# Kernel tuning notes

Hardware: AMD Instinct MI355X
Metric: run time of the kernel (lower is better)

The kernel has to match this reference:

```python
import jax, jax.numpy as jnp
import numpy as np

DECAY = 0.99
EPS_VQ = 1e-5
EPS_LN = 1e-5


def setup_inputs() -> dict:
    key = jax.random.key(0)
    ks = jax.random.split(key, 6)
    N, DIN, D, K = 32768, 1024, 512, 1024
    return {
        "x": jax.random.normal(ks[0], (N, DIN), dtype=jnp.float32),
        "enc_w": jax.random.normal(ks[1], (DIN, D), dtype=jnp.float32) * (1.0 / np.sqrt(DIN)),
        "enc_b": jnp.zeros((D,), jnp.float32),
        "ln_g": jnp.ones((D,), jnp.float32),
        "ln_b": jnp.zeros((D,), jnp.float32),
        "dec_w": jax.random.normal(ks[2], (D, DIN), dtype=jnp.float32) * (1.0 / np.sqrt(D)),
        "dec_b": jnp.zeros((DIN,), jnp.float32),
        "embeddings": jax.random.normal(ks[3], (K, D), dtype=jnp.float32),
        "cluster_size": jnp.ones((K,), jnp.float32),
        "ema_embed_sum": jax.random.normal(ks[4], (K, D), dtype=jnp.float32),
    }


def _layernorm(h, g, b):
    mu = jnp.mean(h, axis=-1, keepdims=True)
    var = jnp.var(h, axis=-1, keepdims=True)
    return (h - mu) * jax.lax.rsqrt(var + EPS_LN) * g + b


def reference(x, enc_w, enc_b, ln_g, ln_b, dec_w, dec_b, embeddings, cluster_size, ema_embed_sum):
    K = embeddings.shape[0]
    # encoder: Linear + LayerNorm
    z_e = _layernorm(x @ enc_w + enc_b, ln_g, ln_b)  # [N, D]
    # pairwise squared L2 distances, expanded GEMM form (same argmin as (z-e)^2.sum)
    d = (jnp.sum(z_e * z_e, axis=1, keepdims=True)
         - 2.0 * (z_e @ embeddings.T)
         + jnp.sum(embeddings * embeddings, axis=1)[None, :])  # [N, K]
    indices = jnp.argmin(d, axis=1)  # [N]
    z_q = embeddings[indices]  # gather [N, D]
    # EMA codebook update (training path; buffers, no grad)
    zd = jax.lax.stop_gradient(z_e)
    counts = jax.ops.segment_sum(jnp.ones_like(indices, jnp.float32), indices, num_segments=K)
    embed_sum = jax.ops.segment_sum(zd, indices, num_segments=K)  # one_hot.T @ z
    new_cluster_size = DECAY * cluster_size + (1.0 - DECAY) * counts
    new_ema_embed_sum = DECAY * ema_embed_sum + (1.0 - DECAY) * embed_sum
    n = jnp.sum(new_cluster_size)
    cs = (new_cluster_size + EPS_VQ) / (n + K * EPS_VQ) * n
    new_embeddings = new_ema_embed_sum / cs[:, None]
    # commitment loss + straight-through estimator
    commit_loss = jnp.mean((z_e - jax.lax.stop_gradient(z_q)) ** 2)
    z_q_st = z_e + jax.lax.stop_gradient(z_q - z_e)
    x_recon = z_q_st @ dec_w + dec_b
    return (x_recon, commit_loss, indices, z_e, z_q_st,
            new_embeddings, new_cluster_size, new_ema_embed_sum)
```

## Files before the change

### kernel.cpp

```cpp
#include <hip/hip_runtime.h>

typedef unsigned long long u64;
typedef unsigned int u32;
typedef _Float16 f16;
typedef _Float16 f16x8 __attribute__((ext_vector_type(8)));
typedef float f32x4 __attribute__((ext_vector_type(4)));

#define MFMA16(a, b, c) __builtin_amdgcn_mfma_f32_16x16x32_f16(a, b, c, 0, 0, 0)

#define NROWS 32768
#define DIN   1024
#define DM    512
#define KC    1024
#define SPLIT_SC  1024.0f
#define SPLIT_INV 0.0009765625f
#define CHSZ  32
#define MAXCH 2048
#define MARGIN 0.5f

#define OFF_XR   0ull
#define OFF_CL   33554432ull
#define OFF_IDX  33554433ull
#define OFF_ZE   33587201ull
#define OFF_ZQ   50364417ull
#define OFF_NE   67141633ull
#define OFF_NCS  67665921ull
#define OFF_NEMA 67666945ull

#define WS_ZNORM   2359296ull
#define WS_IDX     2490368ull
#define WS_COUNTS  2621440ull
#define WS_STARTS  2625536ull
#define WS_OFFW    2629632ull
#define WS_ROWLIST 2633728ull
#define WS_CSD     2764800ull
#define WS_ENORM   2769920ull
#define WS2_CAND   (4ull<<20)
#define WS2_WT1    (36ull<<20)
#define WS2_WT2    (37ull<<20)
#define WS2_DT     (38ull<<20)
#define WS2_E1     (39ull<<20)
#define WS3_CHPFX  (41ull<<20)
#define WS3_CHCODE ((41ull<<20) + 8192)
#define WS3_CPART  ((41ull<<20) + 16384)
#define WS3_PART   ((41ull<<20) + 65536)

__device__ inline void gload16(const f16* g, f16* l) {
  __builtin_amdgcn_global_load_lds((const __attribute__((address_space(1))) void*)g,
                                   (__attribute__((address_space(3))) void*)l, 16, 0, 0);
}

__device__ inline f16x8 ldfrag32(const f16* p, int row, int kc) {
  return *(const f16x8*)(p + row * 32 + ((kc ^ ((row >> 1) & 3)) << 3));
}
__device__ inline f16x8 ldfrag64(const f16* p, int row, int kc) {
  return *(const f16x8*)(p + row * 64 + ((kc ^ (row & 7)) << 3));
}

__device__ inline void stage32(const f16* gbase, int ld, int row0, int k0,
                               f16* lds, int t) {
  int r = t >> 2, c = t & 3;
  int cs = c ^ ((r >> 1) & 3);
  gload16(gbase + (size_t)(row0 + r) * ld + k0 + cs * 8, lds + t * 8);
}

__device__ inline void stage64(const f16* gbase, int ld, int row0, int k0,
                               f16* lds, int t) {
#pragma unroll
  for (int h = 0; h < 2; h++) {
    int e = t + h * 512;
    int r = e >> 3, c = e & 7;
    int cs = c ^ (r & 7);
    gload16(gbase + (size_t)(row0 + r) * ld + k0 + cs * 8, lds + e * 8);
  }
}

#define BAR1_V4   { asm volatile("s_waitcnt vmcnt(4)" ::: "memory"); \
                    __builtin_amdgcn_sched_barrier(0); \
                    __builtin_amdgcn_s_barrier(); \
                    asm volatile("" ::: "memory"); }
#define BAR1_V0L0 { asm volatile("s_waitcnt vmcnt(0) lgkmcnt(0)" ::: "memory"); \
                    __builtin_amdgcn_sched_barrier(0); \
                    __builtin_amdgcn_s_barrier(); \
                    asm volatile("" ::: "memory"); }
#define BAR2      { asm volatile("s_waitcnt lgkmcnt(0)" ::: "memory"); \
                    __builtin_amdgcn_s_barrier(); \
                    asm volatile("" ::: "memory"); }

__device__ inline u32 enc_score(float s) {
  u32 kb = __float_as_uint(s);
  return (kb & 0x80000000u) ? ~kb : (kb | 0x80000000u);
}
__device__ inline float dec_score(u32 u) {
  u32 b = (u & 0x80000000u) ? (u & 0x7fffffffu) : ~u;
  return __uint_as_float(b);
}

__global__ __launch_bounds__(256) void k_init(int* __restrict__ counts) {
  int i = blockIdx.x * 256 + threadIdx.x;
  if (i < KC) counts[i] = 0;
}

__global__ __launch_bounds__(256) void k_prept(const float* __restrict__ W,
                                               f16* __restrict__ o1,
                                               f16* __restrict__ o2,
                                               int K, int N) {
  __shared__ float tile[32][33];
  int tx = threadIdx.x & 31, ty = threadIdx.x >> 5;
  int nb = blockIdx.x * 32, kb = blockIdx.y * 32;
#pragma unroll
  for (int i = 0; i < 32; i += 8)
    tile[ty + i][tx] = W[(size_t)(kb + ty + i) * N + nb + tx];
  __syncthreads();
#pragma unroll
  for (int i = 0; i < 32; i += 8) {
    float v = tile[tx][ty + i];
    f16 h = (f16)v;
    size_t o = (size_t)(nb + ty + i) * K + kb + tx;
    o1[o] = h;
    if (o2) o2[o] = (f16)((v - (float)h) * SPLIT_SC);
  }
}

__global__ __launch_bounds__(256) void k_prepe(const float* __restrict__ E,
                                               f16* __restrict__ e1) {
  int tid = blockIdx.x * 256 + threadIdx.x;
  for (int i = tid; i < KC * DM; i += 131072) e1[i] = (f16)E[i];
}

__global__ __launch_bounds__(64) void k_enorm(const float* __restrict__ E,
                                              float* __restrict__ enorm) {
  int k = blockIdx.x, t = threadIdx.x;
  float s = 0.f;
#pragma unroll
  for (int j = 0; j < 8; j++) {
    float v = E[(size_t)k * DM + t + j * 64];
    s = fmaf(v, v, s);
  }
#pragma unroll
  for (int m = 1; m < 64; m <<= 1) s += __shfl_xor(s, m, 64);
  if (t == 0) enorm[k] = s;
}

__global__ __launch_bounds__(512) void k_genc2(const float* __restrict__ x,
                                               const f16* __restrict__ wt1,
                                               const f16* __restrict__ wt2,
                                               const float* __restrict__ bias,
                                               float* __restrict__ dst) {
  __shared__ __align__(16) f16 A1[128 * 32], A2[128 * 32];
  __shared__ __align__(16) f16 B1[2][128 * 32], B2[2][128 * 32];
  int t = threadIdx.x, lane = t & 63, wid = t >> 6;
  int wm = wid >> 2, wn = wid & 3;
  int l = blockIdx.x;
  int xcd = l & 7, s = l >> 3, ct = s & 3;
  int p = ((s >> 2) << 3) | xcd;
  int m0 = p * 128, n0 = ct * 128;
  int r = t >> 2, cg = t & 3;
  int cslot = cg ^ ((r >> 1) & 3);
  const float* ax = x + (size_t)(m0 + r) * DIN + cg * 8;
  f32x4 accA[4][2] = {}, accB[4][2] = {};

  float4 av0 = *(const float4*)(ax);
  float4 av1 = *(const float4*)(ax + 4);
  stage32(wt1, DIN, n0, 0, B1[0], t);
  stage32(wt2, DIN, n0, 0, B2[0], t);
  int cur = 0;

  for (int it = 0; it < 32; ++it) {
    float4 nv0 = av0, nv1 = av1;
    if (it < 31) {
      int k0n = (it + 1) * 32;
      stage32(wt1, DIN, n0, k0n, B1[cur ^ 1], t);
      stage32(wt2, DIN, n0, k0n, B2[cur ^ 1], t);
      nv0 = *(const float4*)(ax + k0n);
      nv1 = *(const float4*)(ax + k0n + 4);
      asm volatile("s_waitcnt vmcnt(4)" ::: "memory");
    } else {
      asm volatile("s_waitcnt vmcnt(0)" ::: "memory");
    }
    {
      float a[8] = {av0.x, av0.y, av0.z, av0.w, av1.x, av1.y, av1.z, av1.w};
      f16 h1[8], h2[8];
#pragma unroll
      for (int j = 0; j < 8; j++) {
        f16 h = (f16)a[j];
        h1[j] = h;
        h2[j] = (f16)((a[j] - (float)h) * SPLIT_SC);
      }
      *(f16x8*)(A1 + r * 32 + cslot * 8) = *(f16x8*)h1;
      *(f16x8*)(A2 + r * 32 + cslot * 8) = *(f16x8*)h2;
    }
    asm volatile("s_waitcnt lgkmcnt(0)" ::: "memory");
    __builtin_amdgcn_sched_barrier(0);
    __builtin_amdgcn_s_barrier();
    asm volatile("" ::: "memory");
    {
      int kc = lane >> 4;
      f16x8 a1f[4], a2f[4], b1f[2], b2f[2];
#pragma unroll
      for (int m = 0; m < 4; m++) {
        int row = wm * 64 + m * 16 + (lane & 15);
        a1f[m] = ldfrag32(A1, row, kc);
        a2f[m] = ldfrag32(A2, row, kc);
      }
#pragma unroll
      for (int n = 0; n < 2; n++) {
        int row = wn * 32 + n * 16 + (lane & 15);
        b1f[n] = ldfrag32(B1[cur], row, kc);
        b2f[n] = ldfrag32(B2[cur], row, kc);
      }
#pragma unroll
      for (int m = 0; m < 4; m++)
#pragma unroll
        for (int n = 0; n < 2; n++) {
          accA[m][n] = MFMA16(a1f[m], b1f[n], accA[m][n]);
          accB[m][n] = MFMA16(a1f[m], b2f[n], accB[m][n]);
          accB[m][n] = MFMA16(a2f[m], b1f[n], accB[m][n]);
        }
    }
    BAR2;
    av0 = nv0; av1 = nv1; cur ^= 1;
  }
#pragma unroll
  for (int m = 0; m < 4; m++)
#pragma unroll
    for (int n = 0; n < 2; n++)
#pragma unroll
      for (int j = 0; j < 4; j++) {
        int row = m0 + wm * 64 + m * 16 + (lane >> 4) * 4 + j;
        int col = n0 + wn * 32 + n * 16 + (lane & 15);
        dst[(size_t)row * DM + col] = accA[m][n][j] + SPLIT_INV * accB[m][n][j] + bias[col];
      }
}

__global__ __launch_bounds__(512) void k_dist3(const f16* __restrict__ z1,
                                               const f16* __restrict__ e1,
                                               const float* __restrict__ enorm,
                                               u64* __restrict__ cand) {
  __shared__ __align__(16) f16 A1[2][128 * 64], B1[2][128 * 64];
  __shared__ u64 cand_s[128][8];
  int t = threadIdx.x, lane = t & 63, wid = t >> 6;
  int wm = wid >> 2, wn = wid & 3;
  int l = blockIdx.x;
  int xcd = l & 7, s = l >> 3, ct = s & 7;
  int p = ((s >> 3) << 3) | xcd;
  int r0 = p * 128, c0 = ct * 128;
  f32x4 acc[4][2] = {};

  stage64(z1, DM, r0, 0, A1[0], t);
  stage64(e1, DM, c0, 0, B1[0], t);
  int cur = 0;

  for (int it = 0; it < 8; ++it) {
    if (it < 7) {
      int k0n = (it + 1) * 64;
      stage64(z1, DM, r0, k0n, A1[cur ^ 1], t);
      stage64(e1, DM, c0, k0n, B1[cur ^ 1], t);
      BAR1_V4;
    } else {
      BAR1_V0L0;
    }
#pragma unroll
    for (int kk = 0; kk < 2; kk++) {
      int kc = kk * 4 + (lane >> 4);
      f16x8 a1f[4], b1f[2];
#pragma unroll
      for (int m = 0; m < 4; m++)
        a1f[m] = ldfrag64(A1[cur], wm * 64 + m * 16 + (lane & 15), kc);
#pragma unroll
      for (int n = 0; n < 2; n++)
        b1f[n] = ldfrag64(B1[cur], wn * 32 + n * 16 + (lane & 15), kc);
#pragma unroll
      for (int m = 0; m < 4; m++)
#pragma unroll
        for (int n = 0; n < 2; n++) acc[m][n] = MFMA16(a1f[m], b1f[n], acc[m][n]);
    }
    BAR2;
    cur ^= 1;
  }

  float en0 = enorm[c0 + wn * 32 + (lane & 15)];
  float en1 = enorm[c0 + wn * 32 + 16 + (lane & 15)];
#pragma unroll
  for (int m = 0; m < 4; m++)
#pragma unroll
    for (int j = 0; j < 4; j++) {
      int r_l = wm * 64 + m * 16 + (lane >> 4) * 4 + j;
      int col0 = c0 + wn * 32 + (lane & 15);
      float s0 = fmaf(-2.0f, acc[m][0][j], en0);
      float s1 = fmaf(-2.0f, acc[m][1][j], en1);
      u64 k0 = ((u64)enc_score(s0) << 32) | (u32)col0;
      u64 k1 = ((u64)enc_score(s1) << 32) | (u32)(col0 + 16);
      u64 lo = k0 < k1 ? k0 : k1;
      u64 hi = k0 < k1 ? k1 : k0;
#pragma unroll
      for (int msk = 1; msk < 16; msk <<= 1) {
        u64 lo2 = __shfl_xor(lo, msk, 64);
        u64 hi2 = __shfl_xor(hi, msk, 64);
        u64 nlo = lo < lo2 ? lo : lo2;
        u64 losr = lo < lo2 ? lo2 : lo;
        u64 nh = hi < hi2 ? hi : hi2;
        hi = losr < nh ? losr : nh;
        lo = nlo;
      }
      if ((lane & 15) == 0) {
        cand_s[r_l][wn * 2] = lo;
        cand_s[r_l][wn * 2 + 1] = hi;
      }
    }
  __syncthreads();
  if (t < 128) {
    u64 b0 = ~0ull, b1 = ~0ull;
#pragma unroll
    for (int i = 0; i < 8; i++) {
      u64 k = cand_s[t][i];
      if (k < b0) { b1 = b0; b0 = k; }
      else if (k < b1) { b1 = k; }
    }
    u64* dst = cand + ((size_t)(r0 + t) * 16 + ct * 2);
    dst[0] = b0;
    dst[1] = b1;
  }
}

__global__ __launch_bounds__(256) void k_resolve(const u64* __restrict__ cand,
                                                 const float* __restrict__ znorm,
                                                 const float* __restrict__ enorm,
                                                 const float* __restrict__ emb,
                                                 float* __restrict__ out,
                                                 int* __restrict__ idxws,
                                                 int* __restrict__ counts,
                                                 float* __restrict__ cpart) {
  int t = threadIdx.x, bid = blockIdx.x;
  int r0 = bid * 16;
  __shared__ u64 key_s[256];
  __shared__ int idx_s[16];
  __shared__ float commit_s[16];
  __shared__ int flagcnt_s;
  __shared__ int flagrow_s[16];
  key_s[t] = cand[(size_t)r0 * 16 + t];
  if (t == 0) flagcnt_s = 0;
  __syncthreads();

  if (t < 16) {
    u64 best = ~0ull;
#pragma unroll
    for (int i = 0; i < 16; i++) {
      u64 k = key_s[t * 16 + i];
      best = k < best ? k : best;
    }
    float smin = dec_score((u32)(best >> 32));
    float thr = smin + MARGIN;
    int nc = 0;
#pragma unroll
    for (int i = 0; i < 16; i++)
      if (dec_score((u32)(key_s[t * 16 + i] >> 32)) <= thr) nc++;
    idx_s[t] = (int)(u32)(best & 0xffffffffull);
    commit_s[t] = znorm[r0 + t] + smin;
    if (nc > 1) {
      int pz = atomicAdd(&flagcnt_s, 1);
      flagrow_s[pz] = t;
    }
  }
  __syncthreads();

  if (t < 64) {
    int nf = flagcnt_s;
    for (int fi = 0; fi < nf; fi++) {
      int lr = flagrow_s[fi];
      int R = r0 + lr;
      u64 amin = ~0ull;
      for (int i = 0; i < 16; i++) {
        u64 k = key_s[lr * 16 + i];
        amin = k < amin ? k : amin;
      }
      float thr = dec_score((u32)(amin >> 32)) + MARGIN;
      float zn = znorm[R];
      const float* z = out + OFF_ZE + (size_t)R * DM;
      u64 bestk = ~0ull;
      for (int i = 0; i < 16; i++) {
        u64 k = key_s[lr * 16 + i];
        if (dec_score((u32)(k >> 32)) > thr) continue;
        int c = (int)(u32)(k & 0xffffffffull);
        const float* e = emb + (size_t)c * DM;
        float pdot = 0.f;
#pragma unroll
        for (int j = 0; j < 8; j++) pdot = fmaf(z[t + j * 64], e[t + j * 64], pdot);
#pragma unroll
        for (int m = 1; m < 64; m <<= 1) pdot += __shfl_xor(pdot, m, 64);
        float d = fmaf(-2.0f, pdot, zn) + enorm[c];
        u64 pk = ((u64)enc_score(d) << 32) | (u32)c;
        bestk = pk < bestk ? pk : bestk;
      }
      if (t == 0) {
        idx_s[lr] = (int)(u32)(bestk & 0xffffffffull);
        commit_s[lr] = dec_score((u32)(bestk >> 32));
      }
    }
  }
  __syncthreads();

  if (t < 16) {
    int R = r0 + t;
    int idx = idx_s[t];
    out[OFF_IDX + R] = (float)idx;
    idxws[R] = idx;
    atomicAdd(counts + idx, 1);
  }
  __syncthreads();
  for (int rr = 0; rr < 16; rr++) {
    int R = r0 + rr;
    const float* e = emb + (size_t)idx_s[rr] * DM;
    float* zq = out + OFF_ZQ + (size_t)R * DM;
#pragma unroll
    for (int j = 0; j < 2; j++) {
      int c = t + j * 256;
      zq[c] = e[c];
    }
  }
  if (t == 0) {
    float s = 0.f;
#pragma unroll
    for (int i = 0; i < 16; i++) s += commit_s[i];
    cpart[bid] = s;
  }
}

__global__ __launch_bounds__(512) void k_gdec3(const f16* __restrict__ e1,
                                               const int* __restrict__ idxws,
                                               const f16* __restrict__ dT,
                                               const float* __restrict__ bias,
                                               float* __restrict__ dst) {
  __shared__ __align__(16) f16 A1[2][128 * 64], B1[2][128 * 64];
  int t = threadIdx.x, lane = t & 63, wid = t >> 6;
  int wm = wid >> 2, wn = wid & 3;
  int l = blockIdx.x;
  int xcd = l & 7, s = l >> 3, ct = s & 7;
  int p = ((s >> 3) << 3) | xcd;
  int m0 = p * 128, n0 = ct * 128;
  f32x4 acc[4][2] = {};

  int ra = t >> 3;
  int cs = (t & 7) ^ (ra & 7);
  int ia = idxws[m0 + ra];
  int ib = idxws[m0 + 64 + ra];
  const f16* pa = e1 + (size_t)ia * DM + cs * 8;
  const f16* pb = e1 + (size_t)ib * DM + cs * 8;

  gload16(pa, A1[0] + t * 8);
  gload16(pb, A1[0] + (t + 512) * 8);
  stage64(dT, DM, n0, 0, B1[0], t);
  int cur = 0;

  for (int it = 0; it < 8; ++it) {
    if (it < 7) {
      int k0n = (it + 1) * 64;
      gload16(pa + k0n, A1[cur ^ 1] + t * 8);
      gload16(pb + k0n, A1[cur ^ 1] + (t + 512) * 8);
      stage64(dT, DM, n0, k0n, B1[cur ^ 1], t);
      BAR1_V4;
    } else {
      BAR1_V0L0;
    }
#pragma unroll
    for (int kk = 0; kk < 2; kk++) {
      int kc = kk * 4 + (lane >> 4);
      f16x8 a1f[4], b1f[2];
#pragma unroll
      for (int m = 0; m < 4; m++)
        a1f[m] = ldfrag64(A1[cur], wm * 64 + m * 16 + (lane & 15), kc);
#pragma unroll
      for (int n = 0; n < 2; n++)
        b1f[n] = ldfrag64(B1[cur], wn * 32 + n * 16 + (lane & 15), kc);
#pragma unroll
      for (int m = 0; m < 4; m++)
#pragma unroll
        for (int n = 0; n < 2; n++) acc[m][n] = MFMA16(a1f[m], b1f[n], acc[m][n]);
    }
    BAR2;
    cur ^= 1;
  }
#pragma unroll
  for (int m = 0; m < 4; m++)
#pragma unroll
    for (int n = 0; n < 2; n++)
#pragma unroll
      for (int j = 0; j < 4; j++) {
        int row = m0 + wm * 64 + m * 16 + (lane >> 4) * 4 + j;
        int col = n0 + wn * 32 + n * 16 + (lane & 15);
        dst[(size_t)row * DIN + col] = acc[m][n][j] + bias[col];
      }
}

__global__ __launch_bounds__(256) void k_ln3(float* __restrict__ ze,
                                             const float* __restrict__ g,
                                             const float* __restrict__ b,
                                             f16* __restrict__ z1,
                                             float* __restrict__ znorm) {
  int t = threadIdx.x, lane = t & 63, wid = t >> 6;
  int R = blockIdx.x * 4 + wid;
  float* row = ze + (size_t)R * DM;
  float v[8];
  float s = 0.f, sq = 0.f;
#pragma unroll
  for (int j = 0; j < 8; j++) {
    v[j] = row[lane + j * 64];
    s += v[j];
    sq = fmaf(v[j], v[j], sq);
  }
#pragma unroll
  for (int m = 1; m < 64; m <<= 1) {
    s += __shfl_xor(s, m, 64);
    sq += __shfl_xor(sq, m, 64);
  }
  float mu = s * (1.f / DM);
  float var = sq * (1.f / DM) - mu * mu;
  float rs = rsqrtf(var + 1e-5f);
  float zn = 0.f;
#pragma unroll
  for (int j = 0; j < 8; j++) {
    int c = lane + j * 64;
    float o = (v[j] - mu) * rs * g[c] + b[c];
    row[c] = o;
    z1[(size_t)R * DM + c] = (f16)o;
    zn = fmaf(o, o, zn);
  }
#pragma unroll
  for (int m = 1; m < 64; m <<= 1) zn += __shfl_xor(zn, m, 64);
  if (lane == 0) znorm[R] = zn;
}

__global__ __launch_bounds__(1024) void k_scan(const int* __restrict__ counts,
                                               const float* __restrict__ cs_in,
                                               float* __restrict__ out,
                                               int* __restrict__ starts,
                                               int* __restrict__ offw,
                                               float* __restrict__ csd,
                                               const float* __restrict__ cpart,
                                               int* __restrict__ chpfx,
                                               int* __restrict__ chcode) {
  __shared__ float f[1024];
  __shared__ int ib[1024];
  int t = threadIdx.x;
  f[t] = cpart[t] + cpart[t + 1024];
  __syncthreads();
  for (int s = 512; s > 0; s >>= 1) {
    if (t < s) f[t] += f[t + s];
    __syncthreads();
  }
  if (t == 0) out[OFF_CL] = f[0] * (1.f / ((float)NROWS * (float)DM));
  __syncthreads();

  int cnt = counts[t];
  float ncs = 0.99f * cs_in[t] + 0.01f * (float)cnt;
  out[OFF_NCS + t] = ncs;
  f[t] = ncs;
  __syncthreads();
  for (int s = 512; s > 0; s >>= 1) {
    if (t < s) f[t] += f[t + s];
    __syncthreads();
  }
  float n = f[0];
  csd[t] = (ncs + 1e-5f) / (n + (float)KC * 1e-5f) * n;
  ib[t] = cnt;
  __syncthreads();
  for (int s = 1; s < 1024; s <<= 1) {
    int y = (t >= s) ? ib[t - s] : 0;
    __syncthreads();
    ib[t] += y;
    __syncthreads();
  }
  int excl = ib[t] - cnt;
  starts[t] = excl;
  offw[t] = excl;
  int nch = (cnt + CHSZ - 1) / CHSZ;
  __syncthreads();
  ib[t] = nch;
  __syncthreads();
  for (int s = 1; s < 1024; s <<= 1) {
    int y = (t >= s) ? ib[t - s] : 0;
    __syncthreads();
    ib[t] += y;
    __syncthreads();
  }
  int chx = ib[t] - nch;
  chpfx[t] = chx;
  if (t == KC - 1) chpfx[KC] = ib[t];
  for (int j = 0; j < nch; j++) chcode[chx + j] = t;
}

__global__ __launch_bounds__(256) void k_scatter(const int* __restrict__ idxws,
                                                 int* __restrict__ offw,
                                                 int* __restrict__ rowlist) {
  int r = blockIdx.x * 256 + threadIdx.x;
  int idx = idxws[r];
  int pos = atomicAdd(offw + idx, 1);
  rowlist[pos] = r;
}

__global__ __launch_bounds__(128) void k_partsum(const int* __restrict__ chpfx,
                                                 const int* __restrict__ chcode,
                                                 const int* __restrict__ starts,
                                                 const int* __restrict__ counts,
                                                 const int* __restrict__ rowlist,
                                                 const float* __restrict__ out,
                                                 float* __restrict__ part) {
  int c = blockIdx.x, t = threadIdx.x;
  if (c >= chpfx[KC]) return;
  int code = chcode[c];
  int j = c - chpfx[code];
  int ofs = starts[code] + j * CHSZ;
  int len = min(CHSZ, counts[code] - j * CHSZ);
  __shared__ int rl[CHSZ];
  if (t < len) rl[t] = rowlist[ofs + t];
  __syncthreads();
  const float* zeb = out + OFF_ZE;
  float a0 = 0.f, a1 = 0.f, a2 = 0.f, a3 = 0.f;
  for (int i = 0; i < len; i++) {
    const float* z = zeb + (size_t)rl[i] * DM;
    a0 += z[t];
    a1 += z[t + 128];
    a2 += z[t + 256];
    a3 += z[t + 384];
  }
  float* pp = part + (size_t)c * DM;
  pp[t] = a0;
  pp[t + 128] = a1;
  pp[t + 256] = a2;
  pp[t + 384] = a3;
}

__global__ __launch_bounds__(128) void k_codesum2(const int* __restrict__ chpfx,
                                                  const float* __restrict__ part,
                                                  const float* __restrict__ ema_in,
                                                  const float* __restrict__ csd,
                                                  float* __restrict__ out) {
  int k = blockIdx.x, t = threadIdx.x;
  int base = chpfx[k], nch = chpfx[k + 1] - base;
  float a0 = 0.f, a1 = 0.f, a2 = 0.f, a3 = 0.f;
  for (int i = 0; i < nch; i++) {
    const float* pp = part + (size_t)(base + i) * DM;
    a0 += pp[t];
    a1 += pp[t + 128];
    a2 += pp[t + 256];
    a3 += pp[t + 384];
  }
  float cs = csd[k];
  float sum[4] = {a0, a1, a2, a3};
#pragma unroll
  for (int j = 0; j < 4; j++) {
    int c = t + j * 128;
    float e = 0.99f * ema_in[(size_t)k * DM + c] + 0.01f * sum[j];
    out[OFF_NEMA + (size_t)k * DM + c] = e;
    out[OFF_NE + (size_t)k * DM + c] = e / cs;
  }
}

extern "C" void kernel_launch(void* const* d_in, const int* in_sizes, int n_in,
                              void* d_out, int out_size, void* d_ws, size_t ws_size,
                              hipStream_t stream) {
  (void)in_sizes; (void)n_in; (void)out_size; (void)ws_size;
  const float* x = (const float*)d_in[0];
  const float* enc_w = (const float*)d_in[1];
  const float* enc_b = (const float*)d_in[2];
  const float* ln_g = (const float*)d_in[3];
  const float* ln_b = (const float*)d_in[4];
  const float* dec_w = (const float*)d_in[5];
  const float* dec_b = (const float*)d_in[6];
  const float* emb = (const float*)d_in[7];
  const float* cs_in = (const float*)d_in[8];
  const float* ema_in = (const float*)d_in[9];
  float* out = (float*)d_out;
  char* ws = (char*)d_ws;
  float* znorm = (float*)(ws + WS_ZNORM);
  int* idxws = (int*)(ws + WS_IDX);
  int* counts = (int*)(ws + WS_COUNTS);
  int* starts = (int*)(ws + WS_STARTS);
  int* offw = (int*)(ws + WS_OFFW);
  int* rowlist = (int*)(ws + WS_ROWLIST);
  float* csd = (float*)(ws + WS_CSD);
  float* enorm = (float*)(ws + WS_ENORM);
  u64* cand = (u64*)(ws + WS2_CAND);
  f16* wt1 = (f16*)(ws + WS2_WT1);
  f16* wt2 = (f16*)(ws + WS2_WT2);
  f16* dT = (f16*)(ws + WS2_DT);
  f16* e1 = (f16*)(ws + WS2_E1);
  int* chpfx = (int*)(ws + WS3_CHPFX);
  int* chcode = (int*)(ws + WS3_CHCODE);
  float* cpart = (float*)(ws + WS3_CPART);
  float* part = (float*)(ws + WS3_PART);
  f16* z1 = (f16*)out;

  k_init<<<dim3(4), dim3(256), 0, stream>>>(counts);
  k_prept<<<dim3(16, 32), dim3(256), 0, stream>>>(enc_w, wt1, wt2, DIN, DM);
  k_prept<<<dim3(32, 16), dim3(256), 0, stream>>>(dec_w, dT, nullptr, DM, DIN);
  k_prepe<<<dim3(512), dim3(256), 0, stream>>>(emb, e1);
  k_enorm<<<dim3(KC), dim3(64), 0, stream>>>(emb, enorm);
  k_genc2<<<dim3(1024), dim3(512), 0, stream>>>(x, wt1, wt2, enc_b, out + OFF_ZE);
  k_ln3<<<dim3(8192), dim3(256), 0, stream>>>(out + OFF_ZE, ln_g, ln_b, z1, znorm);
  k_dist3<<<dim3(2048), dim3(512), 0, stream>>>(z1, e1, enorm, cand);
  k_resolve<<<dim3(2048), dim3(256), 0, stream>>>(cand, znorm, enorm, emb, out,
                                                  idxws, counts, cpart);
  k_scan<<<dim3(1), dim3(1024), 0, stream>>>(counts, cs_in, out, starts, offw, csd,
                                             cpart, chpfx, chcode);
  k_scatter<<<dim3(NROWS / 256), dim3(256), 0, stream>>>(idxws, offw, rowlist);
  k_partsum<<<dim3(MAXCH), dim3(128), 0, stream>>>(chpfx, chcode, starts, counts,
                                                   rowlist, out, part);
  k_codesum2<<<dim3(KC), dim3(128), 0, stream>>>(chpfx, part, ema_in, csd, out);
  k_gdec3<<<dim3(2048), dim3(512), 0, stream>>>(e1, idxws, dT, dec_b, out + OFF_XR);
}
```

Before: 388.8 us.

## Merge prep kernels into one launch and double-buffer A tiles in encoder GEMM

Five small preparation kernels (counts init, two weight transposes, embedding f16 cast, embedding norms) are folded into a single launch dispatched by block index, which removes launch overhead and gaps between kernels. The encoder GEMM now double-buffers the A (x split-f16) tiles in shared memory and prefetches x two iterations ahead. This lets the f32-to-split-f16 conversion for the next tile overlap with the MFMA work on the current tile and drops one barrier per iteration. It costs extra LDS for the second A buffer, which may affect occupancy, and makes the vmcnt wait logic more intricate.

New measurement: 430.5 us. +10.7%, slower.

```diff
diff --git a/kernel.cpp b/kernel.cpp
--- a/kernel.cpp
+++ b/kernel.cpp
@@ -96,58 +96,69 @@
   return __uint_as_float(b);
 }
 
-__global__ __launch_bounds__(256) void k_init(int* __restrict__ counts) {
-  int i = blockIdx.x * 256 + threadIdx.x;
-  if (i < KC) counts[i] = 0;
-}
-
-__global__ __launch_bounds__(256) void k_prept(const float* __restrict__ W,
-                                               f16* __restrict__ o1,
-                                               f16* __restrict__ o2,
-                                               int K, int N) {
+__global__ __launch_bounds__(256) void k_prep(const float* __restrict__ enc_w,
+                                              const float* __restrict__ dec_w,
+                                              const float* __restrict__ emb,
+                                              f16* __restrict__ wt1,
+                                              f16* __restrict__ wt2,
+                                              f16* __restrict__ dT,
+                                              f16* __restrict__ e1,
+                                              float* __restrict__ enorm,
+                                              int* __restrict__ counts) {
   __shared__ float tile[32][33];
-  int tx = threadIdx.x & 31, ty = threadIdx.x >> 5;
-  int nb = blockIdx.x * 32, kb = blockIdx.y * 32;
-#pragma unroll
-  for (int i = 0; i < 32; i += 8)
-    tile[ty + i][tx] = W[(size_t)(kb + ty + i) * N + nb + tx];
-  __syncthreads();
-#pragma unroll
-  for (int i = 0; i < 32; i += 8) {
-    float v = tile[tx][ty + i];
-    f16 h = (f16)v;
-    size_t o = (size_t)(nb + ty + i) * K + kb + tx;
-    o1[o] = h;
-    if (o2) o2[o] = (f16)((v - (float)h) * SPLIT_SC);
-  }
-}
-
-__global__ __launch_bounds__(256) void k_prepe(const float* __restrict__ E,
-                                               f16* __restrict__ e1) {
-  int tid = blockIdx.x * 256 + threadIdx.x;
-  for (int i = tid; i < KC * DM; i += 131072) e1[i] = (f16)E[i];
-}
-
-__global__ __launch_bounds__(64) void k_enorm(const float* __restrict__ E,
-                                              float* __restrict__ enorm) {
-  int k = blockIdx.x, t = threadIdx.x;
-  float s = 0.f;
-#pragma unroll
-  for (int j = 0; j < 8; j++) {
-    float v = E[(size_t)k * DM + t + j * 64];
-    s = fmaf(v, v, s);
-  }
-#pragma unroll
-  for (int m = 1; m < 64; m <<= 1) s += __shfl_xor(s, m, 64);
-  if (t == 0) enorm[k] = s;
-}
-
-__global__ __launch_bounds__(512) void k_genc2(const float* __restrict__ x,
+  int bid = blockIdx.x, t = threadIdx.x;
+  if (bid < 1024) {
+    const float* W;
+    f16 *o1, *o2;
+    int K, N, bx, by;
+    if (bid < 512) {
+      W = enc_w; o1 = wt1; o2 = wt2; K = DIN; N = DM;
+      bx = bid & 15; by = bid >> 4;
+    } else {
+      int b2 = bid - 512;
+      W = dec_w; o1 = dT; o2 = nullptr; K = DM; N = DIN;
+      bx = b2 & 31; by = b2 >> 5;
+    }
+    int tx = t & 31, ty = t >> 5;
+    int nb = bx * 32, kb = by * 32;
+#pragma unroll
+    for (int i = 0; i < 32; i += 8)
+      tile[ty + i][tx] = W[(size_t)(kb + ty + i) * N + nb + tx];
+    __syncthreads();
+#pragma unroll
+    for (int i = 0; i < 32; i += 8) {
+      float v = tile[tx][ty + i];
+      f16 h = (f16)v;
+      size_t o = (size_t)(nb + ty + i) * K + kb + tx;
+      o1[o] = h;
+      if (o2) o2[o] = (f16)((v - (float)h) * SPLIT_SC);
+    }
+  } else if (bid < 1536) {
+    int tid = (bid - 1024) * 256 + t;
+    for (int i = tid; i < KC * DM; i += 131072) e1[i] = (f16)emb[i];
+  } else if (bid < 1792) {
+    int k = (bid - 1536) * 4 + (t >> 6), lane = t & 63;
+    float s = 0.f;
+#pragma unroll
+    for (int j = 0; j < 8; j++) {
+      float v = emb[(size_t)k * DM + lane + j * 64];
+      s = fmaf(v, v, s);
+    }
+#pragma unroll
+    for (int m = 1; m < 64; m <<= 1) s += __shfl_xor(s, m, 64);
+    if (lane == 0) enorm[k] = s;
+  } else {
+    int i = (bid - 1792) * 256 + t;
+    if (i < KC) counts[i] = 0;
+  }
+}
+
+__global__ __launch_bounds__(512) void k_genc3(const float* __restrict__ x,
                                                const f16* __restrict__ wt1,
                                                const f16* __restrict__ wt2,
                                                const float* __restrict__ bias,
                                                float* __restrict__ dst) {
-  __shared__ __align__(16) f16 A1[128 * 32], A2[128 * 32];
+  __shared__ __align__(16) f16 A1[2][128 * 32], A2[2][128 * 32];
   __shared__ __align__(16) f16 B1[2][128 * 32], B2[2][128 * 32];
   int t = threadIdx.x, lane = t & 63, wid = t >> 6;
   int wm = wid >> 2, wn = wid & 3;
@@ -160,67 +171,77 @@
   const float* ax = x + (size_t)(m0 + r) * DIN + cg * 8;
   f32x4 accA[4][2] = {}, accB[4][2] = {};
 
-  float4 av0 = *(const float4*)(ax);
-  float4 av1 = *(const float4*)(ax + 4);
+#define GCONV(v0, v1, buf)                                                  \
+  {                                                                         \
+    float a_[8] = {v0.x, v0.y, v0.z, v0.w, v1.x, v1.y, v1.z, v1.w};         \
+    f16 h1_[8], h2_[8];                                                     \
+    _Pragma("unroll") for (int j_ = 0; j_ < 8; j_++) {                      \
+      f16 h_ = (f16)a_[j_];                                                 \
+      h1_[j_] = h_;                                                         \
+      h2_[j_] = (f16)((a_[j_] - (float)h_) * SPLIT_SC);                     \
+    }                                                                       \
+    *(f16x8*)(A1[buf] + r * 32 + cslot * 8) = *(f16x8*)h1_;                 \
+    *(f16x8*)(A2[buf] + r * 32 + cslot * 8) = *(f16x8*)h2_;                 \
+  }
+
+#define GCOMP(buf)                                                          \
+  {                                                                         \
+    int kc_ = lane >> 4;                                                    \
+    f16x8 a1f[4], a2f[4], b1f[2], b2f[2];                                   \
+    _Pragma("unroll") for (int m_ = 0; m_ < 4; m_++) {                      \
+      int row_ = wm * 64 + m_ * 16 + (lane & 15);                           \
+      a1f[m_] = ldfrag32(A1[buf], row_, kc_);                               \
+      a2f[m_] = ldfrag32(A2[buf], row_, kc_);                               \
+    }                                                                       \
+    _Pragma("unroll") for (int n_ = 0; n_ < 2; n_++) {                      \
+      int row_ = wn * 32 + n_ * 16 + (lane & 15);                           \
+      b1f[n_] = ldfrag32(B1[buf], row_, kc_);                               \
+      b2f[n_] = ldfrag32(B2[buf], row_, kc_);                               \
+    }                                                                       \
+    _Pragma("unroll") for (int m_ = 0; m_ < 4; m_++)                        \
+      _Pragma("unroll") for (int n_ = 0; n_ < 2; n_++) {                    \
+        accA[m_][n_] = MFMA16(a1f[m_], b1f[n_], accA[m_][n_]);              \
+        accB[m_][n_] = MFMA16(a1f[m_], b2f[n_], accB[m_][n_]);              \
+        accB[m_][n_] = MFMA16(a2f[m_], b1f[n_], accB[m_][n_]);              \
+      }                                                                     \
+  }
+
+  float4 p0 = *(const float4*)(ax);
+  float4 p1 = *(const float4*)(ax + 4);
   stage32(wt1, DIN, n0, 0, B1[0], t);
   stage32(wt2, DIN, n0, 0, B2[0], t);
-  int cur = 0;
+  float4 cv0 = *(const float4*)(ax + 32);
+  float4 cv1 = *(const float4*)(ax + 36);
+  asm volatile("s_waitcnt vmcnt(4)" ::: "memory");
+  GCONV(p0, p1, 0);
+  BAR2;
 
   for (int it = 0; it < 32; ++it) {
-    float4 nv0 = av0, nv1 = av1;
-    if (it < 31) {
-      int k0n = (it + 1) * 32;
-      stage32(wt1, DIN, n0, k0n, B1[cur ^ 1], t);
-      stage32(wt2, DIN, n0, k0n, B2[cur ^ 1], t);
-      nv0 = *(const float4*)(ax + k0n);
-      nv1 = *(const float4*)(ax + k0n + 4);
+    float4 nv0, nv1;
+    if (it + 2 < 32) {
+      nv0 = *(const float4*)(ax + (it + 2) * 32);
+      nv1 = *(const float4*)(ax + (it + 2) * 32 + 4);
+    }
+    if (it + 1 < 32) {
+      stage32(wt1, DIN, n0, (it + 1) * 32, B1[(it + 1) & 1], t);
+      stage32(wt2, DIN, n0, (it + 1) * 32, B2[(it + 1) & 1], t);
+    }
+    if (it <= 29) {
       asm volatile("s_waitcnt vmcnt(4)" ::: "memory");
+    } else if (it == 30) {
+      asm volatile("s_waitcnt vmcnt(2)" ::: "memory");
     } else {
       asm volatile("s_waitcnt vmcnt(0)" ::: "memory");
     }
-    {
-      float a[8] = {av0.x, av0.y, av0.z, av0.w, av1.x, av1.y, av1.z, av1.w};
-      f16 h1[8], h2[8];
-#pragma unroll
-      for (int j = 0; j < 8; j++) {
-        f16 h = (f16)a[j];
-        h1[j] = h;
-        h2[j] = (f16)((a[j] - (float)h) * SPLIT_SC);
-      }
-      *(f16x8*)(A1 + r * 32 + cslot * 8) = *(f16x8*)h1;
-      *(f16x8*)(A2 + r * 32 + cslot * 8) = *(f16x8*)h2;
-    }
-    asm volatile("s_waitcnt lgkmcnt(0)" ::: "memory");
-    __builtin_amdgcn_sched_barrier(0);
-    __builtin_amdgcn_s_barrier();
-    asm volatile("" ::: "memory");
-    {
-      int kc = lane >> 4;
-      f16x8 a1f[4], a2f[4], b1f[2], b2f[2];
-#pragma unroll
-      for (int m = 0; m < 4; m++) {
-        int row = wm * 64 + m * 16 + (lane & 15);
-        a1f[m] = ldfrag32(A1, row, kc);
-        a2f[m] = ldfrag32(A2, row, kc);
-      }
-#pragma unroll
-      for (int n = 0; n < 2; n++) {
-        int row = wn * 32 + n * 16 + (lane & 15);
-        b1f[n] = ldfrag32(B1[cur], row, kc);
-        b2f[n] = ldfrag32(B2[cur], row, kc);
-      }
-#pragma unroll
-      for (int m = 0; m < 4; m++)
-#pragma unroll
-        for (int n = 0; n < 2; n++) {
-          accA[m][n] = MFMA16(a1f[m], b1f[n], accA[m][n]);
-          accB[m][n] = MFMA16(a1f[m], b2f[n], accB[m][n]);
-          accB[m][n] = MFMA16(a2f[m], b1f[n], accB[m][n]);
-        }
-    }
+    if (it + 1 < 32) GCONV(cv0, cv1, (it + 1) & 1);
+    GCOMP(it & 1);
     BAR2;
-    av0 = nv0; av1 = nv1; cur ^= 1;
-  }
+    cv0 = nv0;
+    cv1 = nv1;
+  }
+#undef GCONV
+#undef GCOMP
+
 #pragma unroll
   for (int m = 0; m < 4; m++)
 #pragma unroll
@@ -691,12 +712,9 @@
   float* part = (float*)(ws + WS3_PART);
   f16* z1 = (f16*)out;
 
-  k_init<<<dim3(4), dim3(256), 0, stream>>>(counts);
-  k_prept<<<dim3(16, 32), dim3(256), 0, stream>>>(enc_w, wt1, wt2, DIN, DM);
-  k_prept<<<dim3(32, 16), dim3(256), 0, stream>>>(dec_w, dT, nullptr, DM, DIN);
-  k_prepe<<<dim3(512), dim3(256), 0, stream>>>(emb, e1);
-  k_enorm<<<dim3(KC), dim3(64), 0, stream>>>(emb, enorm);
-  k_genc2<<<dim3(1024), dim3(512), 0, stream>>>(x, wt1, wt2, enc_b, out + OFF_ZE);
+  k_prep<<<dim3(1796), dim3(256), 0, stream>>>(enc_w, dec_w, emb, wt1, wt2, dT,
+                                               e1, enorm, counts);
+  k_genc3<<<dim3(1024), dim3(512), 0, stream>>>(x, wt1, wt2, enc_b, out + OFF_ZE);
   k_ln3<<<dim3(8192), dim3(256), 0, stream>>>(out + OFF_ZE, ln_g, ln_b, z1, znorm);
   k_dist3<<<dim3(2048), dim3(512), 0, stream>>>(z1, e1, enorm, cand);
   k_resolve<<<dim3(2048), dim3(256), 0, stream>>>(cand, znorm, enorm, emb, out,
```
